# Kernel optimization log

Measured on AMD Instinct MI355X. Metric: run time of the kernel, lower is better.

Reference implementation:

```python
import jax, jax.numpy as jnp
import numpy as np

N_CATS = 8
BATCH, SEQ = 2048, 4096


def setup_inputs() -> dict:
    key = jax.random.key(0)
    k1, k2 = jax.random.split(key)
    logits = jax.random.normal(k1, (BATCH, SEQ, N_CATS), dtype=jnp.float32)
    targets = jax.random.randint(k2, (BATCH, SEQ), 0, N_CATS, dtype=jnp.int64)
    return {"logits": logits, "targets": targets}


def _qwk_weights(n_cats, dtype):
    i = jnp.arange(n_cats, dtype=dtype)
    d = i[:, None] - i[None, :]
    return 1.0 - d * d / float((n_cats - 1) ** 2)


def reference(logits, targets):
    n_cats = logits.shape[-1]
    dtype = logits.dtype
    # softmax then argmax (argmax of softmax == argmax of logits, kept faithful)
    probs = jax.nn.softmax(logits, axis=-1)
    preds = jnp.argmax(probs, axis=-1).reshape(-1)          # [B*S]
    t = targets.reshape(-1)                                  # [B*S]
    mask = (t > 0).astype(dtype)                             # masked histogram weights
    n = mask.sum()
    # confusion matrix as a single scatter-add histogram (replaces Python loop)
    cm = jnp.zeros((n_cats, n_cats), dtype).at[t, preds].add(mask)
    cm = cm / n
    marg_true = cm.sum(axis=1)
    marg_pred = cm.sum(axis=0)
    expected = jnp.outer(marg_true, marg_pred)
    w = _qwk_weights(n_cats, dtype)
    num = (w * cm).sum()
    den = (w * expected).sum()
    qwk = jnp.where(den == 0, jnp.zeros((), dtype), num / den)
    qwk = jnp.where(n == 0, jnp.ones((), dtype), qwk)  # n==0 -> loss 0
    return 1.0 - qwk
```

## Files before the change

### kernel.cpp

```cpp
#include <hip/hip_runtime.h>


#define NCATS 8
#define NBINS 64
#define NPART 2048

__global__ __launch_bounds__(256) void qwk_hist_kernel(
    const float* __restrict__ logits,
    const int* __restrict__ targets,
    unsigned int* __restrict__ part,
    int npos)
{
    __shared__ unsigned int lh[NBINS];
    const int tid = threadIdx.x;
    if (tid < NBINS) lh[tid] = 0u;
    __syncthreads();

    const int stride = gridDim.x * blockDim.x;
    for (int pos = blockIdx.x * blockDim.x + tid; pos < npos; pos += stride) {
        const float4* lp = (const float4*)(logits + (size_t)pos * NCATS);
        float4 a = lp[0];
        float4 b = lp[1];
        int best = 0; float bv = a.x;
        if (a.y > bv) { bv = a.y; best = 1; }
        if (a.z > bv) { bv = a.z; best = 2; }
        if (a.w > bv) { bv = a.w; best = 3; }
        if (b.x > bv) { bv = b.x; best = 4; }
        if (b.y > bv) { bv = b.y; best = 5; }
        if (b.z > bv) { bv = b.z; best = 6; }
        if (b.w > bv) { bv = b.w; best = 7; }
        int t = targets[pos];
        if (t > 0) atomicAdd(&lh[t * NCATS + best], 1u);
    }
    __syncthreads();

    if (tid < NBINS) part[blockIdx.x * NBINS + tid] = lh[tid];
}

__global__ __launch_bounds__(256) void qwk_final_kernel(
    const unsigned int* __restrict__ part,
    float* __restrict__ out)
{
    __shared__ unsigned int sums[256];
    __shared__ double cm[NBINS];
    const int t = threadIdx.x;
    const int bin = t & 63;
    const int stripe = t >> 6;
    const int per = NPART / 4;

    unsigned int s = 0;
    #pragma unroll 8
    for (int i = 0; i < per; ++i)
        s += part[(size_t)(stripe * per + i) * NBINS + bin];
    sums[t] = s;
    __syncthreads();

    if (t < NBINS)
        cm[t] = (double)(sums[t] + sums[t + 64] + sums[t + 128] + sums[t + 192]);
    __syncthreads();

    if (t == 0) {
        double n = 0.0;
        #pragma unroll
        for (int i = 0; i < NBINS; ++i) n += cm[i];

        double loss;
        if (n == 0.0) {
            loss = 0.0;
        } else {
            double inv = 1.0 / n;
            double mt[NCATS], mp[NCATS];
            #pragma unroll
            for (int i = 0; i < NCATS; ++i) { mt[i] = 0.0; mp[i] = 0.0; }
            #pragma unroll
            for (int i = 0; i < NCATS; ++i) {
                #pragma unroll
                for (int j = 0; j < NCATS; ++j) {
                    double c = cm[i * NCATS + j] * inv;
                    mt[i] += c;
                    mp[j] += c;
                }
            }
            double num = 0.0, den = 0.0;
            #pragma unroll
            for (int i = 0; i < NCATS; ++i) {
                #pragma unroll
                for (int j = 0; j < NCATS; ++j) {
                    double d = (double)(i - j);
                    double w = 1.0 - d * d / 49.0;
                    num += w * (cm[i * NCATS + j] * inv);
                    den += w * (mt[i] * mp[j]);
                }
            }
            double qwk = (den == 0.0) ? 0.0 : (num / den);
            loss = 1.0 - qwk;
        }
        out[0] = (float)loss;
    }
}

extern "C" void kernel_launch(void* const* d_in, const int* in_sizes, int n_in,
                              void* d_out, int out_size, void* d_ws, size_t ws_size,
                              hipStream_t stream)
{
    const float* logits = (const float*)d_in[0];
    const int* targets = (const int*)d_in[1];
    float* out = (float*)d_out;
    unsigned int* part = (unsigned int*)d_ws;

    const int npos = in_sizes[0] / NCATS;

    qwk_hist_kernel<<<NPART, 256, 0, stream>>>(logits, targets, part, npos);
    qwk_final_kernel<<<1, 256, 0, stream>>>(part, out);
}
```

Before: 385.9 us.

## Fuse histogram and finalize via last-block pattern with per-wave privatized bins

Merges the two kernels into one: each block accumulates into per-wave shared histograms, atomically adds its totals to a global histogram, and the last block to finish computes the loss. Each thread now handles four positions per iteration with vectorized target loads, and the t>0 branch is dropped by zeroing the t==0 row at finalize time. This removes the second launch and the serial partials reduction, and cuts shared-atomic contention, at the cost of a memset, global atomics and a threadfence.

```diff
diff --git a/kernel.cpp b/kernel.cpp
--- a/kernel.cpp
+++ b/kernel.cpp
@@ -3,24 +3,24 @@
 
 #define NCATS 8
 #define NBINS 64
-#define NPART 2048
+#define NBLK  2048
 
-__global__ __launch_bounds__(256) void qwk_hist_kernel(
+__global__ __launch_bounds__(256) void qwk_fused_kernel(
     const float* __restrict__ logits,
     const int* __restrict__ targets,
-    unsigned int* __restrict__ part,
+    unsigned int* __restrict__ ghist,
+    unsigned int* __restrict__ cnt,
+    float* __restrict__ out,
     int npos)
 {
-    __shared__ unsigned int lh[NBINS];
+    __shared__ unsigned int lh[4][NBINS];
     const int tid = threadIdx.x;
-    if (tid < NBINS) lh[tid] = 0u;
+    ((unsigned int*)lh)[tid] = 0u;
     __syncthreads();
 
-    const int stride = gridDim.x * blockDim.x;
-    for (int pos = blockIdx.x * blockDim.x + tid; pos < npos; pos += stride) {
-        const float4* lp = (const float4*)(logits + (size_t)pos * NCATS);
-        float4 a = lp[0];
-        float4 b = lp[1];
+    unsigned int* wh = lh[tid >> 6];
+
+    auto amax = [](const float4& a, const float4& b) -> int {
         int best = 0; float bv = a.x;
         if (a.y > bv) { bv = a.y; best = 1; }
         if (a.z > bv) { bv = a.z; best = 2; }
@@ -29,37 +29,55 @@
         if (b.y > bv) { bv = b.y; best = 5; }
         if (b.z > bv) { bv = b.z; best = 6; }
         if (b.w > bv) { bv = b.w; best = 7; }
-        int t = targets[pos];
-        if (t > 0) atomicAdd(&lh[t * NCATS + best], 1u);
+        return best;
+    };
+
+    const int stride4 = gridDim.x * blockDim.x * 4;
+    int pos = (blockIdx.x * blockDim.x + tid) * 4;
+
+    for (; pos + 3 < npos; pos += stride4) {
+        const float4* lp = (const float4*)(logits + (size_t)pos * NCATS);
+        float4 a0 = lp[0], b0 = lp[1];
+        float4 a1 = lp[2], b1 = lp[3];
+        float4 a2 = lp[4], b2 = lp[5];
+        float4 a3 = lp[6], b3 = lp[7];
+        int4 t4 = *(const int4*)(targets + pos);
+
+        atomicAdd(&wh[(t4.x << 3) | amax(a0, b0)], 1u);
+        atomicAdd(&wh[(t4.y << 3) | amax(a1, b1)], 1u);
+        atomicAdd(&wh[(t4.z << 3) | amax(a2, b2)], 1u);
+        atomicAdd(&wh[(t4.w << 3) | amax(a3, b3)], 1u);
+    }
+    if (pos < npos) {
+        int end = min(pos + 4, npos);
+        for (; pos < end; ++pos) {
+            const float4* lp = (const float4*)(logits + (size_t)pos * NCATS);
+            float4 a = lp[0], b = lp[1];
+            atomicAdd(&wh[(targets[pos] << 3) | amax(a, b)], 1u);
+        }
     }
     __syncthreads();
 
-    if (tid < NBINS) part[blockIdx.x * NBINS + tid] = lh[tid];
-}
-
-__global__ __launch_bounds__(256) void qwk_final_kernel(
-    const unsigned int* __restrict__ part,
-    float* __restrict__ out)
-{
-    __shared__ unsigned int sums[256];
-    __shared__ double cm[NBINS];
-    const int t = threadIdx.x;
-    const int bin = t & 63;
-    const int stripe = t >> 6;
-    const int per = NPART / 4;
-
-    unsigned int s = 0;
-    #pragma unroll 8
-    for (int i = 0; i < per; ++i)
-        s += part[(size_t)(stripe * per + i) * NBINS + bin];
-    sums[t] = s;
+    if (tid < NBINS) {
+        unsigned int s = lh[0][tid] + lh[1][tid] + lh[2][tid] + lh[3][tid];
+        atomicAdd(&ghist[tid], s);
+    }
+    __threadfence();
     __syncthreads();
 
-    if (t < NBINS)
-        cm[t] = (double)(sums[t] + sums[t + 64] + sums[t + 128] + sums[t + 192]);
+    __shared__ unsigned int lastFlag;
+    if (tid == 0)
+        lastFlag = (atomicAdd(cnt, 1u) == (unsigned)gridDim.x - 1u) ? 1u : 0u;
+    __syncthreads();
+    if (!lastFlag) return;
+
+    __shared__ double cm[NBINS];
+    if (tid < NBINS)
+        cm[tid] = (tid < NCATS) ? 0.0
+                                : (double)atomicAdd(&ghist[tid], 0u);
     __syncthreads();
 
-    if (t == 0) {
+    if (tid == 0) {
         double n = 0.0;
         #pragma unroll
         for (int i = 0; i < NBINS; ++i) n += cm[i];
@@ -106,10 +124,11 @@
     const float* logits = (const float*)d_in[0];
     const int* targets = (const int*)d_in[1];
     float* out = (float*)d_out;
-    unsigned int* part = (unsigned int*)d_ws;
+    unsigned int* ghist = (unsigned int*)d_ws;
+    unsigned int* cnt   = ghist + NBINS;
 
     const int npos = in_sizes[0] / NCATS;
 
-    qwk_hist_kernel<<<NPART, 256, 0, stream>>>(logits, targets, part, npos);
-    qwk_final_kernel<<<1, 256, 0, stream>>>(part, out);
+    hipMemsetAsync(d_ws, 0, (NBINS + 1) * sizeof(unsigned int), stream);
+    qwk_fused_kernel<<<NBLK, 256, 0, stream>>>(logits, targets, ghist, cnt, out, npos);
 }
```

Result: slower. 615.5 us (+59.5%).

## Unroll histogram loop four-wide with per-wavefront shared histograms

Applied to the files above, without the earlier changes.

Each thread now issues four independent position loads (logits and targets) per iteration, so more memory requests are in flight at once. The single shared histogram is replaced by one copy per wavefront, which cuts LDS atomic contention; the copies are summed when each block writes its partial result. The t>0 branch is removed, so target-0 counts land in row 0, and the final kernel zeroes that row instead. This trades extra registers and LDS for more memory-level parallelism and fewer conflicting atomics.

```diff
diff --git a/kernel.cpp b/kernel.cpp
--- a/kernel.cpp
+++ b/kernel.cpp
@@ -11,16 +11,14 @@
     unsigned int* __restrict__ part,
     int npos)
 {
-    __shared__ unsigned int lh[NBINS];
+    __shared__ unsigned int lh[4][NBINS];
     const int tid = threadIdx.x;
-    if (tid < NBINS) lh[tid] = 0u;
+    ((unsigned int*)lh)[tid] = 0u;
     __syncthreads();
 
-    const int stride = gridDim.x * blockDim.x;
-    for (int pos = blockIdx.x * blockDim.x + tid; pos < npos; pos += stride) {
-        const float4* lp = (const float4*)(logits + (size_t)pos * NCATS);
-        float4 a = lp[0];
-        float4 b = lp[1];
+    unsigned int* wh = lh[tid >> 6];
+
+    auto amax = [](const float4& a, const float4& b) -> int {
         int best = 0; float bv = a.x;
         if (a.y > bv) { bv = a.y; best = 1; }
         if (a.z > bv) { bv = a.z; best = 2; }
@@ -29,12 +27,42 @@
         if (b.y > bv) { bv = b.y; best = 5; }
         if (b.z > bv) { bv = b.z; best = 6; }
         if (b.w > bv) { bv = b.w; best = 7; }
-        int t = targets[pos];
-        if (t > 0) atomicAdd(&lh[t * NCATS + best], 1u);
+        return best;
+    };
+
+    const int stride = gridDim.x * blockDim.x * 4;
+    int base = blockIdx.x * (blockDim.x * 4) + tid;
+
+    for (; base + 3 * 256 < npos; base += stride) {
+        const float4* lp = (const float4*)logits;
+        float4 a0 = lp[(size_t)(base        ) * 2    ];
+        float4 b0 = lp[(size_t)(base        ) * 2 + 1];
+        float4 a1 = lp[(size_t)(base +  256 ) * 2    ];
+        float4 b1 = lp[(size_t)(base +  256 ) * 2 + 1];
+        float4 a2 = lp[(size_t)(base +  512 ) * 2    ];
+        float4 b2 = lp[(size_t)(base +  512 ) * 2 + 1];
+        float4 a3 = lp[(size_t)(base +  768 ) * 2    ];
+        float4 b3 = lp[(size_t)(base +  768 ) * 2 + 1];
+        int t0 = targets[base];
+        int t1 = targets[base + 256];
+        int t2 = targets[base + 512];
+        int t3 = targets[base + 768];
+
+        atomicAdd(&wh[(t0 << 3) | amax(a0, b0)], 1u);
+        atomicAdd(&wh[(t1 << 3) | amax(a1, b1)], 1u);
+        atomicAdd(&wh[(t2 << 3) | amax(a2, b2)], 1u);
+        atomicAdd(&wh[(t3 << 3) | amax(a3, b3)], 1u);
+    }
+    for (; base < npos; base += 256) {
+        const float4* lp = (const float4*)(logits + (size_t)base * NCATS);
+        float4 a = lp[0], b = lp[1];
+        atomicAdd(&wh[(targets[base] << 3) | amax(a, b)], 1u);
     }
     __syncthreads();
 
-    if (tid < NBINS) part[blockIdx.x * NBINS + tid] = lh[tid];
+    if (tid < NBINS)
+        part[blockIdx.x * NBINS + tid] =
+            lh[0][tid] + lh[1][tid] + lh[2][tid] + lh[3][tid];
 }
 
 __global__ __launch_bounds__(256) void qwk_final_kernel(
@@ -56,7 +84,8 @@
     __syncthreads();
 
     if (t < NBINS)
-        cm[t] = (double)(sums[t] + sums[t + 64] + sums[t + 128] + sums[t + 192]);
+        cm[t] = (t < NCATS) ? 0.0
+              : (double)(sums[t] + sums[t + 64] + sums[t + 128] + sums[t + 192]);
     __syncthreads();
 
     if (t == 0) {
```

New measurement: 388.1 us. No clear change (+0.6%).

## Coalesce logits loads with lane pairs, per-wave histograms, and unmasked atomics

Applied to the files above, without the earlier changes.

Rewrites the histogram kernel so each wave covers 256 positions per iteration. Two lanes split each position's 8 logits as float4 halves, giving fully coalesced nontemporal loads, and combine their argmax with a shuffle. Each wave gets its own shared histogram to cut atomic contention. The t>0 mask moves out of the hot loop and is applied by zeroing row 0 in the final kernel. This adds shuffle work and duplicated lanes, and issues atomics for t==0 positions too.

```diff
diff --git a/kernel.cpp b/kernel.cpp
--- a/kernel.cpp
+++ b/kernel.cpp
@@ -5,36 +5,81 @@
 #define NBINS 64
 #define NPART 2048
 
+typedef float f4 __attribute__((ext_vector_type(4)));
+
 __global__ __launch_bounds__(256) void qwk_hist_kernel(
     const float* __restrict__ logits,
     const int* __restrict__ targets,
     unsigned int* __restrict__ part,
     int npos)
 {
-    __shared__ unsigned int lh[NBINS];
+    __shared__ unsigned int lh[4][NBINS];
     const int tid = threadIdx.x;
-    if (tid < NBINS) lh[tid] = 0u;
+    ((unsigned int*)lh)[tid] = 0u;
     __syncthreads();
 
-    const int stride = gridDim.x * blockDim.x;
-    for (int pos = blockIdx.x * blockDim.x + tid; pos < npos; pos += stride) {
-        const float4* lp = (const float4*)(logits + (size_t)pos * NCATS);
-        float4 a = lp[0];
-        float4 b = lp[1];
-        int best = 0; float bv = a.x;
-        if (a.y > bv) { bv = a.y; best = 1; }
-        if (a.z > bv) { bv = a.z; best = 2; }
-        if (a.w > bv) { bv = a.w; best = 3; }
-        if (b.x > bv) { bv = b.x; best = 4; }
-        if (b.y > bv) { bv = b.y; best = 5; }
-        if (b.z > bv) { bv = b.z; best = 6; }
-        if (b.w > bv) { bv = b.w; best = 7; }
-        int t = targets[pos];
-        if (t > 0) atomicAdd(&lh[t * NCATS + best], 1u);
+    unsigned int* wh = lh[tid >> 6];
+    const int wv    = tid >> 6;
+    const int lane  = tid & 63;
+    const int half  = lane & 1;
+    const int pairk = lane >> 1;
+
+    const f4* lp = (const f4*)logits;
+
+    const int stride = gridDim.x * 1024;
+    int Pw = blockIdx.x * 1024 + wv * 256;
+
+    for (; Pw + 256 <= npos; Pw += stride) {
+        f4  f[8];
+        int tg[8];
+        #pragma unroll
+        for (int j = 0; j < 8; ++j)
+            f[j] = __builtin_nontemporal_load(&lp[(size_t)Pw * 2 + j * 64 + lane]);
+        #pragma unroll
+        for (int j = 0; j < 8; ++j)
+            tg[j] = __builtin_nontemporal_load(&targets[Pw + j * 32 + pairk]);
+
+        #pragma unroll
+        for (int j = 0; j < 8; ++j) {
+            f4 a = f[j];
+            int bi = half << 2; float bv = a.x;
+            if (a.y > bv) { bv = a.y; bi = (half << 2) | 1; }
+            if (a.z > bv) { bv = a.z; bi = (half << 2) | 2; }
+            if (a.w > bv) { bv = a.w; bi = (half << 2) | 3; }
+            float obv = __shfl_xor(bv, 1);
+            int   obi = __shfl_xor(bi, 1);
+            float lov = half ? obv : bv;  int loi = half ? obi : bi;
+            float hiv = half ? bv : obv;  int hii = half ? bi : obi;
+            int best = (hiv > lov) ? hii : loi;
+            if (!half) atomicAdd(&wh[(tg[j] << 3) | best], 1u);
+        }
+    }
+
+    for (; Pw < npos; Pw += stride) {
+        #pragma unroll
+        for (int j = 0; j < 8; ++j) {
+            int p = Pw + j * 32 + pairk;
+            if (p < npos) {
+                f4 a = lp[(size_t)p * 2 + half];
+                int t = targets[p];
+                int bi = half << 2; float bv = a.x;
+                if (a.y > bv) { bv = a.y; bi = (half << 2) | 1; }
+                if (a.z > bv) { bv = a.z; bi = (half << 2) | 2; }
+                if (a.w > bv) { bv = a.w; bi = (half << 2) | 3; }
+                float obv = __shfl_xor(bv, 1);
+                int   obi = __shfl_xor(bi, 1);
+                float lov = half ? obv : bv;  int loi = half ? obi : bi;
+                float hiv = half ? bv : obv;  int hii = half ? bi : obi;
+                int best = (hiv > lov) ? hii : loi;
+                if (!half) atomicAdd(&wh[(t << 3) | best], 1u);
+            }
+        }
     }
     __syncthreads();
 
-    if (tid < NBINS) part[blockIdx.x * NBINS + tid] = lh[tid];
+    if (tid < NBINS)
+        part[blockIdx.x * NBINS + tid] =
+            lh[0][tid] + lh[1][tid] + lh[2][tid] + lh[3][tid];
 }
 
 __global__ __launch_bounds__(256) void qwk_final_kernel(
@@ -56,7 +101,8 @@
     __syncthreads();
 
     if (t < NBINS)
-        cm[t] = (double)(sums[t] + sums[t + 64] + sums[t + 128] + sums[t + 192]);
+        cm[t] = (t < NCATS) ? 0.0
+              : (double)(sums[t] + sums[t + 64] + sums[t + 128] + sums[t + 192]);
     __syncthreads();
 
     if (t == 0) {
```

New measurement: 362.6 us. 1.06x faster.
